# Kernel tuning notes

Measured on AMD Instinct MI355X. Metric: run time of the kernel, lower is better.

The kernel has to match this reference:

```python
import jax, jax.numpy as jnp
import numpy as np

NX, NY = 4096, 4096
T = 1.0
TIME_STEPS = 400
DT = T / TIME_STEPS
DX = 1.0 / (NX - 1)
DY = 1.0 / (NY - 1)
Z = 1.0
FROG = 2
BC = jnp.array([-1.0, 1.0], dtype=jnp.float32)


def _conv_ax0(A, f):
    # valid cross-correlation along axis 0 (matches F.conv1d after transpose)
    L = f.shape[0]
    n = A.shape[0] - L + 1
    out = f[0] * A[0:n, :]
    for k in range(1, L):
        out = out + f[k] * A[k:k + n, :]
    return out


def _conv_ax1(A, f):
    L = f.shape[0]
    n = A.shape[1] - L + 1
    out = f[0] * A[:, 0:n]
    for k in range(1, L):
        out = out + f[k] * A[:, k:k + n]
    return out


def _amper(E, Hx, Hy, f, s):
    # S1: d/dx of Hy ; S2: d/dy of Hx
    S1 = (Z * DT / DX) * _conv_ax0(Hy, f)[0:-1, s:NY - s]
    S2 = (Z * DT / DY) * _conv_ax1(Hx, f)[s:NX - s, 0:-1]
    return E[s:NX - s, s:NY - s] + S1 - S2


def _faraday(E, Hx, Hy, f, s):
    S3 = (DT / (Z * DY)) * _conv_ax1(E, f)[s:NX - s, :]
    S4 = (DT / (Z * DX)) * _conv_ax0(E, f)[:, s:NY - s]
    Ax = Hx[s:NX - s, s - 1:NY - s] - S3
    Ay = Hy[s - 1:NX - s, s:NY - s] + S4
    return Ax, Ay


def setup_inputs() -> dict:
    key = jax.random.key(0)
    k1, k2, k3 = jax.random.split(key, 3)
    X1 = jax.random.normal(k1, (NX, NY), dtype=jnp.float32)
    X2 = jax.random.normal(k2, (NX, NY), dtype=jnp.float32)
    X3 = jax.random.normal(k3, (NX, NY), dtype=jnp.float32)
    w1 = jnp.ones((1,), dtype=jnp.float32)
    return {"X1": X1, "X2": X2, "X3": X3, "w1": w1}


def reference(X1, X2, X3, w1):
    f4 = jnp.concatenate([(w1 - 1.0) / 3.0, -w1, w1, (1.0 - w1) / 3.0])
    E, Hx, Hy = X1, X2, X3
    # boundary-order then interior (frog) Ampere update of E
    E = E.at[1:NX - 1, 1:NY - 1].set(_amper(X1, X2, X3, BC, 1))
    E = E.at[FROG:NX - FROG, FROG:NY - FROG].set(_amper(E, X2, X3, f4, FROG))
    # Faraday updates of Hx, Hy from the ORIGINAL fields (bc order)
    Ax1, Ay1 = _faraday(X1, X2, X3, BC, 1)
    Hx = Hx.at[1:NX - 1, 0:NY - 1].set(Ax1)
    Hy = Hy.at[0:NX - 1, 1:NY - 1].set(Ay1)
    # interior Faraday updates using updated E, Hx, Hy
    Ax2, Ay2 = _faraday(E, Hx, Hy, f4, FROG)
    Hx = Hx.at[FROG:NX - FROG, FROG - 1:NY - FROG].set(Ax2)
    Hy = Hy.at[FROG - 1:NX - FROG, FROG:NY - FROG].set(Ay2)
    return (E, Hx, Hy)
```

## Files before the change

### kernel.cpp

```cpp
#include <hip/hip_runtime.h>

#define NXg 4096
#define NYg 4096
#define BROWS 12
#define ROW0 8
#define NBANDS 340
#define NPANEL 16
#define CCOLS 256
#define LCOLS 264
#define R3 18
#define R2 15
#define R1 15
#define CPR 66
#define NCHUNK 3168
#define NJ 13
#define NSLOTF 13312

static constexpr float C = 10.2375f;

struct F4  { float v[4];  };
struct F7  { float v[7];  };
struct F10 { float v[10]; };

__device__ __forceinline__ F4 lb4(const float* Lrow, int lc) {
    const float4 b = *(const float4*)(Lrow + lc);
    F4 x; x.v[0] = b.x; x.v[1] = b.y; x.v[2] = b.z; x.v[3] = b.w;
    return x;
}
__device__ __forceinline__ F7 l7(const float* Lrow, int lc) {
    const float4 a = *(const float4*)(Lrow + lc - 4);
    const float4 b = *(const float4*)(Lrow + lc);
    const float4 c = *(const float4*)(Lrow + lc + 4);
    F7 x;
    x.v[0] = a.w; x.v[1] = b.x; x.v[2] = b.y; x.v[3] = b.z;
    x.v[4] = b.w; x.v[5] = c.x; x.v[6] = c.y;
    return x;
}
__device__ __forceinline__ F10 l10(const float* Lrow, int lc) {
    const float4 a = *(const float4*)(Lrow + lc - 4);
    const float4 b = *(const float4*)(Lrow + lc);
    const float4 c = *(const float4*)(Lrow + lc + 4);
    F10 x;
    x.v[0] = a.y; x.v[1] = a.z; x.v[2] = a.w;
    x.v[3] = b.x; x.v[4] = b.y; x.v[5] = b.z; x.v[6] = b.w;
    x.v[7] = c.x; x.v[8] = c.y; x.v[9] = c.z;
    return x;
}
__device__ __forceinline__ F4 mid(const F7& s) {
    F4 x; x.v[0] = s.v[1]; x.v[1] = s.v[2]; x.v[2] = s.v[3]; x.v[3] = s.v[4];
    return x;
}

__global__ __launch_bounds__(256) void band_kernel(
    const float* __restrict__ X1, const float* __restrict__ X2,
    const float* __restrict__ X3, const float* __restrict__ w1,
    float* __restrict__ E, float* __restrict__ Hx, float* __restrict__ Hy)
{
    __shared__ __attribute__((aligned(16))) float B[NSLOTF];

    const int tid  = threadIdx.x;
    const int col0 = blockIdx.x * CCOLS;
    const int i0   = ROW0 + blockIdx.y * BROWS;

    const float wv = w1[0];
    const float f0 = (wv - 1.0f) / 3.0f;
    const float f1 = -wv;
    const float f2 = wv;
    const float f3 = (1.0f - wv) / 3.0f;

    const int cq = tid & 63;
    const int g  = tid >> 6;
    const int lc = 4 + 4 * cq;
    const bool gL = (blockIdx.x == 0) && (cq == 0);
    const bool gR = (blockIdx.x == NPANEL - 1) && (cq == 63);

    {
        #pragma unroll
        for (int j = 0; j < NJ; ++j) {
            const int c    = j * 256 + tid;
            const int cc2  = (c < NCHUNK) ? c : (NCHUNK - 1);
            const int row  = cc2 / CPR;
            const int col4 = cc2 - row * CPR;
            const float* base = (row < R3) ? X3 : ((row < R3 + R2) ? X2 : X1);
            const int grow = i0 + ((row < R3) ? (row - 3)
                                 : ((row < R3 + R2) ? (row - R3 - 1)
                                                    : (row - R3 - R2 - 1)));
            const float* gp = base + (size_t)grow * NYg + (col0 - 4) + col4 * 4;
            float* lp = B + j * 1024 + (tid >> 6) * 256;
            __builtin_amdgcn_global_load_lds(
                (const __attribute__((address_space(1))) void*)gp,
                (__attribute__((address_space(3))) void*)lp, 16, 0, 0);
        }
    }
    __syncthreads();

    const float* T3 = B;
    const float* T2 = B + R3 * LCOLS;
    const float* T1 = B + (R3 + R2) * LCOLS;

    auto eRow4 = [&](const F4& a, const F4& b, const F4& cc, const F4& d,
                     const F10& x2r, const F4& x1r) -> F4 {
        F4 e;
        #pragma unroll
        for (int q = 0; q < 4; ++q) {
            const float e1 = x1r.v[q] + C * (cc.v[q] - b.v[q])
                                      - C * (x2r.v[q + 3] - x2r.v[q + 2]);
            e.v[q] = e1
                + C * (f0 * a.v[q] + f1 * b.v[q] + f2 * cc.v[q] + f3 * d.v[q])
                - C * (f0 * x2r.v[q + 1] + f1 * x2r.v[q + 2]
                     + f2 * x2r.v[q + 3] + f3 * x2r.v[q + 4]);
        }
        if (gL) {
            e.v[0] = x1r.v[0];
            e.v[1] = x1r.v[1] + C * (cc.v[1] - b.v[1])
                              - C * (x2r.v[4] - x2r.v[3]);
        }
        if (gR) {
            e.v[3] = x1r.v[3];
            e.v[2] = x1r.v[2] + C * (cc.v[2] - b.v[2])
                              - C * (x2r.v[5] - x2r.v[4]);
        }
        return e;
    };

    auto computeRow = [&](int r) {
        const int i = i0 + r;

        const F4  x3m3 = lb4(&T3[(r    ) * LCOLS], lc);
        const F7  x3m2 = l7 (&T3[(r + 1) * LCOLS], lc);
        const F7  x3m1 = l7 (&T3[(r + 2) * LCOLS], lc);
        const F7  x3i  = l7 (&T3[(r + 3) * LCOLS], lc);
        const F7  x3p1 = l7 (&T3[(r + 4) * LCOLS], lc);
        const F4  x3p2 = lb4(&T3[(r + 5) * LCOLS], lc);
        const F4  x3p3 = lb4(&T3[(r + 6) * LCOLS], lc);

        const F10 x2m1 = l10(&T2[(r    ) * LCOLS], lc);
        const F10 x2i  = l10(&T2[(r + 1) * LCOLS], lc);
        const F10 x2p1 = l10(&T2[(r + 2) * LCOLS], lc);
        const F10 x2p2 = l10(&T2[(r + 3) * LCOLS], lc);

        const F4  x1m1 = lb4(&T1[(r    ) * LCOLS], lc);
        const F7  x1i  = l7 (&T1[(r + 1) * LCOLS], lc);
        const F4  x1p1 = lb4(&T1[(r + 2) * LCOLS], lc);
        const F4  x1p2 = lb4(&T1[(r + 3) * LCOLS], lc);

        F7 e7;
        #pragma unroll
        for (int m = 0; m < 7; ++m) {
            const float e1 = x1i.v[m] + C * (x3i.v[m] - x3m1.v[m])
                                      - C * (x2i.v[m + 2] - x2i.v[m + 1]);
            e7.v[m] = e1
                + C * (f0 * x3m2.v[m] + f1 * x3m1.v[m] + f2 * x3i.v[m] + f3 * x3p1.v[m])
                - C * (f0 * x2i.v[m] + f1 * x2i.v[m + 1] + f2 * x2i.v[m + 2] + f3 * x2i.v[m + 3]);
        }
        if (gL) {
            e7.v[1] = x1i.v[1];
            e7.v[2] = x1i.v[2] + C * (x3i.v[2] - x3m1.v[2])
                               - C * (x2i.v[4] - x2i.v[3]);
        }
        if (gR) {
            e7.v[4] = x1i.v[4];
            e7.v[3] = x1i.v[3] + C * (x3i.v[3] - x3m1.v[3])
                               - C * (x2i.v[5] - x2i.v[4]);
        }

        const F4 em1 = eRow4(x3m3,      mid(x3m2), mid(x3m1), mid(x3i), x2m1, x1m1);
        const F4 ep1 = eRow4(mid(x3m1), mid(x3i),  mid(x3p1), x3p2,     x2p1, x1p1);
        const F4 ep2 = eRow4(mid(x3i),  mid(x3p1), x3p2,      x3p3,     x2p2, x1p2);

        float hx[4], hy[4];
        #pragma unroll
        for (int q = 0; q < 4; ++q) {
            hx[q] = x2i.v[q + 3] - C * (x1i.v[q + 2] - x1i.v[q + 1])
                  - C * (f0 * e7.v[q] + f1 * e7.v[q + 1]
                       + f2 * e7.v[q + 2] + f3 * e7.v[q + 3]);
            hy[q] = x3i.v[q + 1] + C * (x1p1.v[q] - x1i.v[q + 1])
                  + C * (f0 * em1.v[q] + f1 * e7.v[q + 1]
                       + f2 * ep1.v[q] + f3 * ep2.v[q]);
        }
        if (gL) {
            hx[0] = x2i.v[3] - C * (x1i.v[2] - x1i.v[1]);
            hy[0] = x3i.v[1];
            hy[1] = x3i.v[2] + C * (x1p1.v[1] - x1i.v[2]);
        }
        if (gR) {
            hx[3] = x2i.v[6];
            hy[3] = x3i.v[4];
            hx[2] = x2i.v[5] - C * (x1i.v[4] - x1i.v[3]);
            hy[2] = x3i.v[3] + C * (x1p1.v[2] - x1i.v[3]);
        }

        const size_t idx = (size_t)i * NYg + col0 + 4 * cq;
        *(float4*)(E  + idx) = make_float4(e7.v[1], e7.v[2], e7.v[3], e7.v[4]);
        *(float4*)(Hx + idx) = make_float4(hx[0], hx[1], hx[2], hx[3]);
        *(float4*)(Hy + idx) = make_float4(hy[0], hy[1], hy[2], hy[3]);
    };

    computeRow(g);
    computeRow(g + 4);
    computeRow(g + 8);
}

#define TRE 8
#define EROWSE 12
#define ECOLSE 136

__global__ __launch_bounds__(256) void edge_kernel(
    const float* __restrict__ X1, const float* __restrict__ X2,
    const float* __restrict__ X3, const float* __restrict__ w1,
    float* __restrict__ E, float* __restrict__ Hx, float* __restrict__ Hy)
{
    __shared__ float elds[EROWSE][ECOLSE];
    const int t    = threadIdx.x;
    const int row0 = blockIdx.y ? (NXg - TRE) : 0;
    const int col0 = blockIdx.x * 128;

    const float wv = w1[0];
    const float f0 = (wv - 1.0f) / 3.0f;
    const float f1 = -wv;
    const float f2 = wv;
    const float f3 = (1.0f - wv) / 3.0f;

    for (int cidx = t; cidx < EROWSE * ECOLSE; cidx += 256) {
        const int r  = cidx / ECOLSE;
        const int cc = cidx - r * ECOLSE;
        const int gr = row0 - 2 + r;
        const int gc = col0 - 4 + cc;
        float e = 0.0f;
        if (gr >= 0 && gr < NXg && gc >= 0 && gc < NYg) {
            const size_t idx = (size_t)gr * NYg + gc;
            const float x1 = X1[idx];
            if (gr == 0 || gr == NXg - 1 || gc == 0 || gc == NYg - 1) {
                e = x1;
            } else {
                float e1 = x1 + C * (X3[idx] - X3[idx - NYg])
                              - C * (X2[idx] - X2[idx - 1]);
                if (gr >= 2 && gr <= NXg - 3 && gc >= 2 && gc <= NYg - 3) {
                    e1 += C * (f0 * X3[idx - 2 * NYg] + f1 * X3[idx - NYg]
                             + f2 * X3[idx] + f3 * X3[idx + NYg])
                        - C * (f0 * X2[idx - 2] + f1 * X2[idx - 1]
                             + f2 * X2[idx] + f3 * X2[idx + 1]);
                }
                e = e1;
            }
        }
        elds[r][cc] = e;
    }
    __syncthreads();

    for (int cidx = t; cidx < TRE * 128; cidx += 256) {
        const int hr  = cidx >> 7;
        const int tc  = cidx & 127;
        const int gr  = row0 + hr;
        const int gcc = col0 + tc;
        const size_t idx = (size_t)gr * NYg + gcc;
        const int lr  = hr + 2;
        const int lc2 = tc + 4;

        const float ec = elds[lr][lc2];
        E[idx] = ec;

        const float x1 = X1[idx];

        float hx = X2[idx];
        if (gr >= 1 && gr <= NXg - 2 && gcc <= NYg - 2)
            hx -= C * (X1[idx + 1] - x1);
        if (gr >= 2 && gr <= NXg - 3 && gcc >= 1 && gcc <= NYg - 3) {
            hx -= C * (f0 * elds[lr][lc2 - 1] + f1 * ec
                     + f2 * elds[lr][lc2 + 1] + f3 * elds[lr][lc2 + 2]);
        }
        Hx[idx] = hx;

        float hy = X3[idx];
        if (gr <= NXg - 2 && gcc >= 1 && gcc <= NYg - 2)
            hy += C * (X1[idx + NYg] - x1);
        if (gr >= 1 && gr <= NXg - 3 && gcc >= 2 && gcc <= NYg - 3) {
            hy += C * (f0 * elds[lr - 1][lc2] + f1 * ec
                     + f2 * elds[lr + 1][lc2] + f3 * elds[lr + 2][lc2]);
        }
        Hy[idx] = hy;
    }
}

extern "C" void kernel_launch(void* const* d_in, const int* in_sizes, int n_in,
                              void* d_out, int out_size, void* d_ws, size_t ws_size,
                              hipStream_t stream) {
    const float* X1 = (const float*)d_in[0];
    const float* X2 = (const float*)d_in[1];
    const float* X3 = (const float*)d_in[2];
    const float* w1 = (const float*)d_in[3];

    float* E  = (float*)d_out;
    float* Hx = (float*)d_out + (size_t)NXg * NYg;
    float* Hy = (float*)d_out + 2 * (size_t)NXg * NYg;

    edge_kernel<<<dim3(32, 2), 256, 0, stream>>>(X1, X2, X3, w1, E, Hx, Hy);
    band_kernel<<<dim3(NPANEL, NBANDS), 256, 0, stream>>>(X1, X2, X3, w1, E, Hx, Hy);
}
```

Measured before the change: 98.59 us.

## Fuse edge and band kernels, interleave LDS rows, staged waitcnt pipelining

Result: no change. 99.02 us (+0.4%).

```diff
diff --git a/kernel.cpp b/kernel.cpp
--- a/kernel.cpp
+++ b/kernel.cpp
@@ -8,15 +8,14 @@
 #define NPANEL 16
 #define CCOLS 256
 #define LCOLS 264
-#define R3 18
-#define R2 15
-#define R1 15
 #define CPR 66
 #define NCHUNK 3168
 #define NJ 13
 #define NSLOTF 13312
 
 static constexpr float C = 10.2375f;
+
+typedef float v4f __attribute__((ext_vector_type(4)));
 
 struct F4  { float v[4];  };
 struct F7  { float v[7];  };
@@ -50,8 +49,12 @@
     F4 x; x.v[0] = s.v[1]; x.v[1] = s.v[2]; x.v[2] = s.v[3]; x.v[3] = s.v[4];
     return x;
 }
-
-__global__ __launch_bounds__(256) void band_kernel(
+__device__ __forceinline__ void nt_store4(float* p, float a, float b, float c, float d) {
+    v4f v; v.x = a; v.y = b; v.z = c; v.w = d;
+    __builtin_nontemporal_store(v, (v4f*)p);
+}
+
+__global__ __launch_bounds__(256) void fused_kernel(
     const float* __restrict__ X1, const float* __restrict__ X2,
     const float* __restrict__ X3, const float* __restrict__ w1,
     float* __restrict__ E, float* __restrict__ Hx, float* __restrict__ Hy)
@@ -60,13 +63,80 @@
 
     const int tid  = threadIdx.x;
     const int col0 = blockIdx.x * CCOLS;
-    const int i0   = ROW0 + blockIdx.y * BROWS;
-
-    const float wv = w1[0];
-    const float f0 = (wv - 1.0f) / 3.0f;
-    const float f1 = -wv;
-    const float f2 = wv;
-    const float f3 = (1.0f - wv) / 3.0f;
+
+    float wv = w1[0];
+    float f0 = (wv - 1.0f) / 3.0f;
+    float f1 = -wv;
+    float f2 = wv;
+    float f3 = (1.0f - wv) / 3.0f;
+    asm volatile("" : "+v"(f0), "+v"(f1), "+v"(f2), "+v"(f3));
+
+    if (blockIdx.y >= NBANDS) {
+        const int row0 = (blockIdx.y == NBANDS) ? 0 : (NXg - 8);
+
+        for (int cidx = tid; cidx < 12 * LCOLS; cidx += 256) {
+            const int r  = cidx / LCOLS;
+            const int cc = cidx - r * LCOLS;
+            const int gr = row0 - 2 + r;
+            const int gc = col0 - 4 + cc;
+            float e = 0.0f;
+            if (gr >= 0 && gr < NXg && gc >= 0 && gc < NYg) {
+                const size_t idx = (size_t)gr * NYg + gc;
+                const float x1 = X1[idx];
+                if (gr == 0 || gr == NXg - 1 || gc == 0 || gc == NYg - 1) {
+                    e = x1;
+                } else {
+                    float e1 = x1 + C * (X3[idx] - X3[idx - NYg])
+                                  - C * (X2[idx] - X2[idx - 1]);
+                    if (gr >= 2 && gr <= NXg - 3 && gc >= 2 && gc <= NYg - 3) {
+                        e1 += C * (f0 * X3[idx - 2 * NYg] + f1 * X3[idx - NYg]
+                                 + f2 * X3[idx] + f3 * X3[idx + NYg])
+                            - C * (f0 * X2[idx - 2] + f1 * X2[idx - 1]
+                                 + f2 * X2[idx] + f3 * X2[idx + 1]);
+                    }
+                    e = e1;
+                }
+            }
+            B[r * LCOLS + cc] = e;
+        }
+        __syncthreads();
+
+        for (int cidx = tid; cidx < 8 * CCOLS; cidx += 256) {
+            const int hr  = cidx >> 8;
+            const int tc  = cidx & (CCOLS - 1);
+            const int gr  = row0 + hr;
+            const int gcc = col0 + tc;
+            const size_t idx = (size_t)gr * NYg + gcc;
+            const int lr  = hr + 2;
+            const int lc2 = tc + 4;
+
+            const float ec = B[lr * LCOLS + lc2];
+            E[idx] = ec;
+
+            const float x1 = X1[idx];
+
+            float hx = X2[idx];
+            if (gr >= 1 && gr <= NXg - 2 && gcc <= NYg - 2)
+                hx -= C * (X1[idx + 1] - x1);
+            if (gr >= 2 && gr <= NXg - 3 && gcc >= 1 && gcc <= NYg - 3) {
+                hx -= C * (f0 * B[lr * LCOLS + lc2 - 1] + f1 * ec
+                         + f2 * B[lr * LCOLS + lc2 + 1] + f3 * B[lr * LCOLS + lc2 + 2]);
+            }
+            Hx[idx] = hx;
+
+            float hy = X3[idx];
+            if (gr <= NXg - 2 && gcc >= 1 && gcc <= NYg - 2)
+                hy += C * (X1[idx + NYg] - x1);
+            if (gr >= 1 && gr <= NXg - 3 && gcc >= 2 && gcc <= NYg - 3) {
+                hy += C * (f0 * B[(lr - 1) * LCOLS + lc2] + f1 * ec
+                         + f2 * B[(lr + 1) * LCOLS + lc2] + f3 * B[(lr + 2) * LCOLS + lc2]);
+            }
+            Hy[idx] = hy;
+        }
+        return;
+    }
+
+    const int i0 = ROW0 + blockIdx.y * BROWS;
 
     const int cq = tid & 63;
     const int g  = tid >> 6;
@@ -79,12 +149,19 @@
         for (int j = 0; j < NJ; ++j) {
             const int c    = j * 256 + tid;
             const int cc2  = (c < NCHUNK) ? c : (NCHUNK - 1);
-            const int row  = cc2 / CPR;
-            const int col4 = cc2 - row * CPR;
-            const float* base = (row < R3) ? X3 : ((row < R3 + R2) ? X2 : X1);
-            const int grow = i0 + ((row < R3) ? (row - 3)
-                                 : ((row < R3 + R2) ? (row - R3 - 1)
-                                                    : (row - R3 - R2 - 1)));
+            const int t    = cc2 / CPR;
+            const int col4 = cc2 - t * CPR;
+            const float* base;
+            int grow;
+            if (t < 45) {
+                const int k = t / 3;
+                const int m = t - 3 * k;
+                base = (m == 0) ? X3 : ((m == 1) ? X2 : X1);
+                grow = i0 + ((m == 0) ? (k - 3) : (k - 1));
+            } else {
+                base = X3;
+                grow = i0 + (t - 33);
+            }
             const float* gp = base + (size_t)grow * NYg + (col0 - 4) + col4 * 4;
             float* lp = B + j * 1024 + (tid >> 6) * 256;
             __builtin_amdgcn_global_load_lds(
@@ -92,11 +169,10 @@
                 (__attribute__((address_space(3))) void*)lp, 16, 0, 0);
         }
     }
-    __syncthreads();
-
-    const float* T3 = B;
-    const float* T2 = B + R3 * LCOLS;
-    const float* T1 = B + (R3 + R2) * LCOLS;
+
+    auto T3row = [&](int k) { return B + ((k <= 14) ? 3 * k : 30 + k) * LCOLS; };
+    auto T2row = [&](int k) { return B + (3 * k + 1) * LCOLS; };
+    auto T1row = [&](int k) { return B + (3 * k + 2) * LCOLS; };
 
     auto eRow4 = [&](const F4& a, const F4& b, const F4& cc, const F4& d,
                      const F10& x2r, const F4& x1r) -> F4 {
@@ -126,23 +202,23 @@
     auto computeRow = [&](int r) {
         const int i = i0 + r;
 
-        const F4  x3m3 = lb4(&T3[(r    ) * LCOLS], lc);
-        const F7  x3m2 = l7 (&T3[(r + 1) * LCOLS], lc);
-        const F7  x3m1 = l7 (&T3[(r + 2) * LCOLS], lc);
-        const F7  x3i  = l7 (&T3[(r + 3) * LCOLS], lc);
-        const F7  x3p1 = l7 (&T3[(r + 4) * LCOLS], lc);
-        const F4  x3p2 = lb4(&T3[(r + 5) * LCOLS], lc);
-        const F4  x3p3 = lb4(&T3[(r + 6) * LCOLS], lc);
-
-        const F10 x2m1 = l10(&T2[(r    ) * LCOLS], lc);
-        const F10 x2i  = l10(&T2[(r + 1) * LCOLS], lc);
-        const F10 x2p1 = l10(&T2[(r + 2) * LCOLS], lc);
-        const F10 x2p2 = l10(&T2[(r + 3) * LCOLS], lc);
-
-        const F4  x1m1 = lb4(&T1[(r    ) * LCOLS], lc);
-        const F7  x1i  = l7 (&T1[(r + 1) * LCOLS], lc);
-        const F4  x1p1 = lb4(&T1[(r + 2) * LCOLS], lc);
-        const F4  x1p2 = lb4(&T1[(r + 3) * LCOLS], lc);
+        const F4  x3m3 = lb4(T3row(r    ), lc);
+        const F7  x3m2 = l7 (T3row(r + 1), lc);
+        const F7  x3m1 = l7 (T3row(r + 2), lc);
+        const F7  x3i  = l7 (T3row(r + 3), lc);
+        const F7  x3p1 = l7 (T3row(r + 4), lc);
+        const F4  x3p2 = lb4(T3row(r + 5), lc);
+        const F4  x3p3 = lb4(T3row(r + 6), lc);
+
+        const F10 x2m1 = l10(T2row(r    ), lc);
+        const F10 x2i  = l10(T2row(r + 1), lc);
+        const F10 x2p1 = l10(T2row(r + 2), lc);
+        const F10 x2p2 = l10(T2row(r + 3), lc);
+
+        const F4  x1m1 = lb4(T1row(r    ), lc);
+        const F7  x1i  = l7 (T1row(r + 1), lc);
+        const F4  x1p1 = lb4(T1row(r + 2), lc);
+        const F4  x1p2 = lb4(T1row(r + 3), lc);
 
         F7 e7;
         #pragma unroll
@@ -191,95 +267,20 @@
         }
 
         const size_t idx = (size_t)i * NYg + col0 + 4 * cq;
-        *(float4*)(E  + idx) = make_float4(e7.v[1], e7.v[2], e7.v[3], e7.v[4]);
-        *(float4*)(Hx + idx) = make_float4(hx[0], hx[1], hx[2], hx[3]);
-        *(float4*)(Hy + idx) = make_float4(hy[0], hy[1], hy[2], hy[3]);
+        nt_store4(E  + idx, e7.v[1], e7.v[2], e7.v[3], e7.v[4]);
+        nt_store4(Hx + idx, hx[0], hx[1], hx[2], hx[3]);
+        nt_store4(Hy + idx, hy[0], hy[1], hy[2], hy[3]);
     };
 
+    asm volatile("s_waitcnt vmcnt(5)" ::: "memory");
+    __builtin_amdgcn_s_barrier();
     computeRow(g);
+    asm volatile("s_waitcnt vmcnt(5)" ::: "memory");
+    __builtin_amdgcn_s_barrier();
     computeRow(g + 4);
+    asm volatile("s_waitcnt vmcnt(6)" ::: "memory");
+    __builtin_amdgcn_s_barrier();
     computeRow(g + 8);
-}
-
-#define TRE 8
-#define EROWSE 12
-#define ECOLSE 136
-
-__global__ __launch_bounds__(256) void edge_kernel(
-    const float* __restrict__ X1, const float* __restrict__ X2,
-    const float* __restrict__ X3, const float* __restrict__ w1,
-    float* __restrict__ E, float* __restrict__ Hx, float* __restrict__ Hy)
-{
-    __shared__ float elds[EROWSE][ECOLSE];
-    const int t    = threadIdx.x;
-    const int row0 = blockIdx.y ? (NXg - TRE) : 0;
-    const int col0 = blockIdx.x * 128;
-
-    const float wv = w1[0];
-    const float f0 = (wv - 1.0f) / 3.0f;
-    const float f1 = -wv;
-    const float f2 = wv;
-    const float f3 = (1.0f - wv) / 3.0f;
-
-    for (int cidx = t; cidx < EROWSE * ECOLSE; cidx += 256) {
-        const int r  = cidx / ECOLSE;
-        const int cc = cidx - r * ECOLSE;
-        const int gr = row0 - 2 + r;
-        const int gc = col0 - 4 + cc;
-        float e = 0.0f;
-        if (gr >= 0 && gr < NXg && gc >= 0 && gc < NYg) {
-            const size_t idx = (size_t)gr * NYg + gc;
-            const float x1 = X1[idx];
-            if (gr == 0 || gr == NXg - 1 || gc == 0 || gc == NYg - 1) {
-                e = x1;
-            } else {
-                float e1 = x1 + C * (X3[idx] - X3[idx - NYg])
-                              - C * (X2[idx] - X2[idx - 1]);
-                if (gr >= 2 && gr <= NXg - 3 && gc >= 2 && gc <= NYg - 3) {
-                    e1 += C * (f0 * X3[idx - 2 * NYg] + f1 * X3[idx - NYg]
-                             + f2 * X3[idx] + f3 * X3[idx + NYg])
-                        - C * (f0 * X2[idx - 2] + f1 * X2[idx - 1]
-                             + f2 * X2[idx] + f3 * X2[idx + 1]);
-                }
-                e = e1;
-            }
-        }
-        elds[r][cc] = e;
-    }
-    __syncthreads();
-
-    for (int cidx = t; cidx < TRE * 128; cidx += 256) {
-        const int hr  = cidx >> 7;
-        const int tc  = cidx & 127;
-        const int gr  = row0 + hr;
-        const int gcc = col0 + tc;
-        const size_t idx = (size_t)gr * NYg + gcc;
-        const int lr  = hr + 2;
-        const int lc2 = tc + 4;
-
-        const float ec = elds[lr][lc2];
-        E[idx] = ec;
-
-        const float x1 = X1[idx];
-
-        float hx = X2[idx];
-        if (gr >= 1 && gr <= NXg - 2 && gcc <= NYg - 2)
-            hx -= C * (X1[idx + 1] - x1);
-        if (gr >= 2 && gr <= NXg - 3 && gcc >= 1 && gcc <= NYg - 3) {
-            hx -= C * (f0 * elds[lr][lc2 - 1] + f1 * ec
-                     + f2 * elds[lr][lc2 + 1] + f3 * elds[lr][lc2 + 2]);
-        }
-        Hx[idx] = hx;
-
-        float hy = X3[idx];
-        if (gr <= NXg - 2 && gcc >= 1 && gcc <= NYg - 2)
-            hy += C * (X1[idx + NYg] - x1);
-        if (gr >= 1 && gr <= NXg - 3 && gcc >= 2 && gcc <= NYg - 3) {
-            hy += C * (f0 * elds[lr - 1][lc2] + f1 * ec
-                     + f2 * elds[lr + 1][lc2] + f3 * elds[lr + 2][lc2]);
-        }
-        Hy[idx] = hy;
-    }
 }
 
 extern "C" void kernel_launch(void* const* d_in, const int* in_sizes, int n_in,
@@ -294,6 +295,6 @@
     float* Hx = (float*)d_out + (size_t)NXg * NYg;
     float* Hy = (float*)d_out + 2 * (size_t)NXg * NYg;
 
-    edge_kernel<<<dim3(32, 2), 256, 0, stream>>>(X1, X2, X3, w1, E, Hx, Hy);
-    band_kernel<<<dim3(NPANEL, NBANDS), 256, 0, stream>>>(X1, X2, X3, w1, E, Hx, Hy);
-}
+    fused_kernel<<<dim3(NPANEL, NBANDS + 2), 256, 0, stream>>>(
+        X1, X2, X3, w1, E, Hx, Hy);
+}
```
